# Kernel optimization log

Measured on AMD Instinct MI355X. Metric: run time of the kernel, lower is better.

## Reference

```python
import jax, jax.numpy as jnp
import numpy as np


def setup_inputs() -> dict:
    key = jax.random.key(0)
    k1, k2, k3, k4, k5 = jax.random.split(key, 5)
    num_chunks, input_dim, output_dim = 100000, 256, 512
    num_members, num_cells = 400000, 50000
    chunk_features = jax.random.normal(k1, (num_chunks, input_dim), dtype=jnp.float32)
    member_idx = jax.random.randint(k2, (num_members,), 0, num_chunks, dtype=jnp.int32)
    segment_ids = jnp.sort(jax.random.randint(k3, (num_members,), 0, num_cells, dtype=jnp.int32))
    W = jax.random.normal(k4, (input_dim, output_dim), dtype=jnp.float32) / np.sqrt(input_dim)
    b = jax.random.normal(k5, (output_dim,), dtype=jnp.float32) * 0.01
    return {
        "chunk_features": chunk_features,
        "member_idx": member_idx,
        "segment_ids": segment_ids,
        "num_cells": num_cells,
        "W": W,
        "b": b,
    }


def reference(chunk_features, member_idx, segment_ids, num_cells, W, b):
    # Gather per-membership chunk embeddings: (M, D)
    gathered = jnp.take(chunk_features, member_idx, axis=0)
    # Segment-sum over cells, then divide by counts -> segment mean (num_cells, D)
    sums = jax.ops.segment_sum(gathered, segment_ids, num_segments=num_cells)
    counts = jax.ops.segment_sum(
        jnp.ones((member_idx.shape[0],), dtype=chunk_features.dtype),
        segment_ids, num_segments=num_cells)
    cell_emb = sums / jnp.maximum(counts, 1.0)[:, None]
    # Linear projection (input_dim != output_dim)
    return cell_emb @ W + b
```

## Files before the change

### kernel.cpp

```cpp
#include <hip/hip_runtime.h>

typedef __attribute__((ext_vector_type(8))) short short8;
typedef __attribute__((ext_vector_type(4))) float floatx4;

static __device__ __forceinline__ unsigned short f2bf(float f) {
    unsigned int u = __float_as_uint(f);
    u = (u + 0x7FFFu + ((u >> 16) & 1u)) >> 16;
    return (unsigned short)u;
}

__global__ void starts_kernel(const int* __restrict__ seg, int M, int num_cells,
                              int* __restrict__ starts) {
    int m = blockIdx.x * blockDim.x + threadIdx.x;
    if (m > M) return;
    int prev = (m == 0) ? -1 : seg[m - 1];
    int cur  = (m == M) ? num_cells : seg[m];
    for (int c = prev + 1; c <= cur; ++c) starts[c] = m;
}

__global__ void prep_wt_kernel(const float* __restrict__ W,
                               unsigned short* __restrict__ Wt) {
    int g = blockIdx.x * blockDim.x + threadIdx.x;
    int n = g >> 8;
    int k = g & 255;
    Wt[g] = f2bf(W[k * 512 + n]);
}

__global__ __launch_bounds__(256) void seg_mean_kernel(
        const float* __restrict__ chunk_features,
        const int* __restrict__ member_idx,
        const int* __restrict__ starts,
        int num_cells,
        unsigned short* __restrict__ cell_emb) {
    const int wid  = threadIdx.x >> 6;
    const int lane = threadIdx.x & 63;
    const int c = blockIdx.x * 4 + wid;

    float4 acc = make_float4(0.f, 0.f, 0.f, 0.f);
    int cnt = 0;

    if (c < num_cells) {
        const int s = starts[c];
        const int e = starts[c + 1];
        cnt = e - s;
        const float4* cf = (const float4*)chunk_features;

        for (int base = s; base < e; base += 64) {
            int m = base + lane;
            int idx = (m < e) ? member_idx[m] : 0;
            int n = e - base; if (n > 64) n = 64;
            for (int j0 = 0; j0 < n; j0 += 8) {
                int k = n - j0; if (k > 8) k = 8;
                float4 v[8];
#pragma unroll
                for (int j = 0; j < 8; ++j) {
                    if (j < k) {
                        int ci = __shfl(idx, j0 + j);
                        v[j] = cf[(size_t)ci * 64 + lane];
                    }
                }
#pragma unroll
                for (int j = 0; j < 8; ++j) {
                    if (j < k) {
                        acc.x += v[j].x; acc.y += v[j].y;
                        acc.z += v[j].z; acc.w += v[j].w;
                    }
                }
            }
        }
    }

    float inv = 1.0f / (float)(cnt > 0 ? cnt : 1);
    ushort4 o;
    o.x = f2bf(acc.x * inv);
    o.y = f2bf(acc.y * inv);
    o.z = f2bf(acc.z * inv);
    o.w = f2bf(acc.w * inv);
    *(ushort4*)(cell_emb + (size_t)c * 256 + lane * 4) = o;
}

__global__ __launch_bounds__(256) void gemm_kernel(
        const unsigned short* __restrict__ A,
        const unsigned short* __restrict__ Bt,
        const float* __restrict__ bias,
        float* __restrict__ out,
        int Mreal) {
    constexpr int LDSS = 40;
    __shared__ unsigned short As[128 * LDSS];
    __shared__ unsigned short Bs[128 * LDSS];

    const int tid  = threadIdx.x;
    const int wid  = tid >> 6;
    const int lane = tid & 63;
    const int wm = wid & 1, wn = wid >> 1;
    const int l15 = lane & 15, q = lane >> 4;
    const int m0 = blockIdx.y * 128;
    const int n0 = blockIdx.x * 128;

    floatx4 acc[4][4] = {};

    for (int kb = 0; kb < 256; kb += 32) {
#pragma unroll
        for (int r = 0; r < 2; ++r) {
            int chunk = tid + r * 256;
            int row = chunk >> 2;
            int col = (chunk & 3) * 8;
            *(short8*)&As[row * LDSS + col] =
                *(const short8*)&A[(size_t)(m0 + row) * 256 + kb + col];
            *(short8*)&Bs[row * LDSS + col] =
                *(const short8*)&Bt[(size_t)(n0 + row) * 256 + kb + col];
        }
        __syncthreads();

        short8 af[4], bf[4];
#pragma unroll
        for (int mi = 0; mi < 4; ++mi)
            af[mi] = *(const short8*)&As[(wm * 64 + mi * 16 + l15) * LDSS + q * 8];
#pragma unroll
        for (int ni = 0; ni < 4; ++ni)
            bf[ni] = *(const short8*)&Bs[(wn * 64 + ni * 16 + l15) * LDSS + q * 8];
#pragma unroll
        for (int mi = 0; mi < 4; ++mi)
#pragma unroll
            for (int ni = 0; ni < 4; ++ni)
                acc[mi][ni] = __builtin_amdgcn_mfma_f32_16x16x32_bf16(
                    af[mi], bf[ni], acc[mi][ni], 0, 0, 0);
        __syncthreads();
    }

#pragma unroll
    for (int ni = 0; ni < 4; ++ni) {
        int n = n0 + wn * 64 + ni * 16 + l15;
        float bv = bias[n];
#pragma unroll
        for (int mi = 0; mi < 4; ++mi) {
            int mbase = m0 + wm * 64 + mi * 16 + q * 4;
#pragma unroll
            for (int r = 0; r < 4; ++r) {
                int row = mbase + r;
                if (row < Mreal)
                    out[(size_t)row * 512 + n] = acc[mi][ni][r] + bv;
            }
        }
    }
}

extern "C" void kernel_launch(void* const* d_in, const int* in_sizes, int n_in,
                              void* d_out, int out_size, void* d_ws, size_t ws_size,
                              hipStream_t stream) {
    const float* chunk_features = (const float*)d_in[0];
    const int*   member_idx     = (const int*)d_in[1];
    const int*   segment_ids    = (const int*)d_in[2];
    const float* W              = (const float*)d_in[4];
    const float* bias           = (const float*)d_in[5];
    float* out = (float*)d_out;

    const int M        = in_sizes[1];
    const int out_dim  = in_sizes[5];
    const int num_cells = out_size / out_dim;
    const int mtiles = (num_cells + 127) / 128;
    const int Mpad   = mtiles * 128;

    unsigned short* cell_emb = (unsigned short*)d_ws;
    unsigned short* Wt       = cell_emb + (size_t)Mpad * 256;
    int*            starts   = (int*)(Wt + 512 * 256);

    hipLaunchKernelGGL(starts_kernel, dim3((M + 1 + 255) / 256), dim3(256), 0, stream,
                       segment_ids, M, num_cells, starts);
    hipLaunchKernelGGL(prep_wt_kernel, dim3(512), dim3(256), 0, stream, W, Wt);
    hipLaunchKernelGGL(seg_mean_kernel, dim3(Mpad / 4), dim3(256), 0, stream,
                       chunk_features, member_idx, starts, num_cells, cell_emb);
    hipLaunchKernelGGL(gemm_kernel, dim3(4, mtiles), dim3(256), 0, stream,
                       cell_emb, Wt, bias, out, num_cells);
}
```

Before: 282.4 us.

## Pre-cast chunk features to bf16 and gather half-width rows; fuse prep kernels

Adds a pass that converts the whole fp32 chunk_features table to bf16 in workspace. The segment-mean kernel then gathers 512-byte bf16 rows instead of 1 KB fp32 rows and widens them to fp32 for accumulation. The starts computation, the W transpose-cast and the new cast are merged into one launch using block-range dispatch. The aim is to halve the bytes moved by the random gather. The cost is an extra full read and write of the table each call, plus bf16 rounding of the inputs before summation.

```diff
diff --git a/kernel.cpp b/kernel.cpp
--- a/kernel.cpp
+++ b/kernel.cpp
@@ -8,26 +8,51 @@
     u = (u + 0x7FFFu + ((u >> 16) & 1u)) >> 16;
     return (unsigned short)u;
 }
-
-__global__ void starts_kernel(const int* __restrict__ seg, int M, int num_cells,
-                              int* __restrict__ starts) {
-    int m = blockIdx.x * blockDim.x + threadIdx.x;
-    if (m > M) return;
-    int prev = (m == 0) ? -1 : seg[m - 1];
-    int cur  = (m == M) ? num_cells : seg[m];
-    for (int c = prev + 1; c <= cur; ++c) starts[c] = m;
-}
-
-__global__ void prep_wt_kernel(const float* __restrict__ W,
-                               unsigned short* __restrict__ Wt) {
-    int g = blockIdx.x * blockDim.x + threadIdx.x;
-    int n = g >> 8;
-    int k = g & 255;
-    Wt[g] = f2bf(W[k * 512 + n]);
+static __device__ __forceinline__ float bf2f(unsigned short h) {
+    return __uint_as_float(((unsigned int)h) << 16);
+}
+
+__global__ __launch_bounds__(256) void prep_kernel(
+        const float* __restrict__ cf, int cast_elems,
+        const int* __restrict__ seg, int M, int num_cells,
+        const float* __restrict__ W,
+        unsigned short* __restrict__ cf16,
+        int* __restrict__ starts,
+        unsigned short* __restrict__ Wt,
+        int castB, int startB) {
+    const int b = blockIdx.x;
+    const int tid = threadIdx.x;
+    if (b < castB) {
+        int g = (b * 256 + tid) * 8;
+        if (g + 8 <= cast_elems) {
+            float4 a = *(const float4*)(cf + g);
+            float4 c = *(const float4*)(cf + g + 4);
+            short8 o;
+            o[0] = (short)f2bf(a.x); o[1] = (short)f2bf(a.y);
+            o[2] = (short)f2bf(a.z); o[3] = (short)f2bf(a.w);
+            o[4] = (short)f2bf(c.x); o[5] = (short)f2bf(c.y);
+            o[6] = (short)f2bf(c.z); o[7] = (short)f2bf(c.w);
+            *(short8*)(cf16 + g) = o;
+        } else {
+            for (int i = g; i < cast_elems; ++i) cf16[i] = f2bf(cf[i]);
+        }
+    } else if (b < castB + startB) {
+        int m = (b - castB) * 256 + tid;
+        if (m > M) return;
+        int prev = (m == 0) ? -1 : seg[m - 1];
+        int cur  = (m == M) ? num_cells : seg[m];
+        for (int c = prev + 1; c <= cur; ++c) starts[c] = m;
+    } else {
+        int g = (b - castB - startB) * 256 + tid;
+        if (g < 512 * 256) {
+            int n = g >> 8, k = g & 255;
+            Wt[g] = f2bf(W[k * 512 + n]);
+        }
+    }
 }
 
 __global__ __launch_bounds__(256) void seg_mean_kernel(
-        const float* __restrict__ chunk_features,
+        const unsigned short* __restrict__ cf16,
         const int* __restrict__ member_idx,
         const int* __restrict__ starts,
         int num_cells,
@@ -43,7 +68,6 @@
         const int s = starts[c];
         const int e = starts[c + 1];
         cnt = e - s;
-        const float4* cf = (const float4*)chunk_features;
 
         for (int base = s; base < e; base += 64) {
             int m = base + lane;
@@ -51,19 +75,19 @@
             int n = e - base; if (n > 64) n = 64;
             for (int j0 = 0; j0 < n; j0 += 8) {
                 int k = n - j0; if (k > 8) k = 8;
-                float4 v[8];
+                ushort4 v[8];
 #pragma unroll
                 for (int j = 0; j < 8; ++j) {
                     if (j < k) {
                         int ci = __shfl(idx, j0 + j);
-                        v[j] = cf[(size_t)ci * 64 + lane];
+                        v[j] = *(const ushort4*)(cf16 + (size_t)ci * 256 + lane * 4);
                     }
                 }
 #pragma unroll
                 for (int j = 0; j < 8; ++j) {
                     if (j < k) {
-                        acc.x += v[j].x; acc.y += v[j].y;
-                        acc.z += v[j].z; acc.w += v[j].w;
+                        acc.x += bf2f(v[j].x); acc.y += bf2f(v[j].y);
+                        acc.z += bf2f(v[j].z); acc.w += bf2f(v[j].w);
                     }
                 }
             }
@@ -155,21 +179,27 @@
     const float* bias           = (const float*)d_in[5];
     float* out = (float*)d_out;
 
-    const int M        = in_sizes[1];
-    const int out_dim  = in_sizes[5];
-    const int num_cells = out_size / out_dim;
+    const int cast_elems = in_sizes[0];
+    const int M          = in_sizes[1];
+    const int out_dim    = in_sizes[5];
+    const int num_cells  = out_size / out_dim;
     const int mtiles = (num_cells + 127) / 128;
     const int Mpad   = mtiles * 128;
 
     unsigned short* cell_emb = (unsigned short*)d_ws;
     unsigned short* Wt       = cell_emb + (size_t)Mpad * 256;
-    int*            starts   = (int*)(Wt + 512 * 256);
-
-    hipLaunchKernelGGL(starts_kernel, dim3((M + 1 + 255) / 256), dim3(256), 0, stream,
-                       segment_ids, M, num_cells, starts);
-    hipLaunchKernelGGL(prep_wt_kernel, dim3(512), dim3(256), 0, stream, W, Wt);
+    unsigned short* cf16     = Wt + 512 * 256;
+    int*            starts   = (int*)(cf16 + (((size_t)cast_elems + 7) & ~7ull));
+
+    const int castB  = (cast_elems + 2047) / 2048;
+    const int startB = (M + 1 + 255) / 256;
+    const int wtB    = (512 * 256 + 255) / 256;
+
+    hipLaunchKernelGGL(prep_kernel, dim3(castB + startB + wtB), dim3(256), 0, stream,
+                       chunk_features, cast_elems, segment_ids, M, num_cells, W,
+                       cf16, starts, Wt, castB, startB);
     hipLaunchKernelGGL(seg_mean_kernel, dim3(Mpad / 4), dim3(256), 0, stream,
-                       chunk_features, member_idx, starts, num_cells, cell_emb);
+                       cf16, member_idx, starts, num_cells, cell_emb);
     hipLaunchKernelGGL(gemm_kernel, dim3(4, mtiles), dim3(256), 0, stream,
                        cell_emb, Wt, bias, out, num_cells);
 }
```

Measured after the change: 280.9 us. No clear change (-0.5%).
